# Kernel tuning notes

Hardware: AMD Instinct MI355X
Metric: run time of the kernel (lower is better)

Reference implementation:

```python
import jax, jax.numpy as jnp
import numpy as np

SEQ_LEN = 4096
N_FEAT = 2048
N_PADD = 128


def setup_inputs() -> dict:
    key = jax.random.key(0)
    kx, kw = jax.random.split(key)
    x = jax.random.normal(kx, (SEQ_LEN, N_FEAT), dtype=jnp.float32)
    # Fused QKV dense: features = 3 * n_feat
    W = jax.random.normal(kw, (N_FEAT, 3 * N_FEAT), dtype=jnp.float32) * (1.0 / np.sqrt(N_FEAT))
    b = jnp.zeros((3 * N_FEAT,), dtype=jnp.float32)
    return {"x": x, "W": W, "b": b, "n_padd": N_PADD}


def reference(x, W, b, n_padd):
    # Fused QKV projection, split along feature axis (as in nn.Dense + jnp.split)
    qkv = x @ W + b  # [S, 3F]
    q, k, v = jnp.split(qkv, 3, axis=1)  # each [S, F]
    S, F = q.shape
    idx = jnp.arange(S)
    # scores[i, j] = q_i . k_j / sqrt(F)
    scores = (q @ k.T) * (1.0 / jnp.sqrt(jnp.float32(F)))  # [S, S]
    seq_mask = idx >= n_padd                      # valid (non-padding) positions
    causal = idx[None, :] <= idx[:, None]         # j <= i
    mask = causal & seq_mask[None, :]             # kernel: causal_mask & seq_mask
    row_valid = seq_mask                          # rows < n_padd are not computed/stored
    neg_inf = jnp.float32(-jnp.inf)
    scores = jnp.where(mask, scores, neg_inf)
    # Fully-masked (padding) rows would softmax to NaN; neutralize then zero output.
    scores = jnp.where(row_valid[:, None], scores, 0.0)
    att = jax.nn.softmax(scores, axis=-1)         # row-wise stable softmax
    out = att @ v                                 # [S, F]
    out = jnp.where(row_valid[:, None], out, 0.0)  # padded rows produce zeros
    return out
```

## Files before the change

### kernel.cpp

```cpp
#include <hip/hip_runtime.h>
#include <cstdint>
#include <cstddef>
#include <cmath>

typedef unsigned short u16;
typedef short v8s __attribute__((ext_vector_type(8)));
typedef float v4f __attribute__((ext_vector_type(4)));

constexpr int SEQ = 4096;
constexpr int FEAT = 2048;
constexpr int F3 = 6144;


__device__ __forceinline__ u16 f2bf(float f) {
  union { float f; uint32_t u; } v; v.f = f;
  uint32_t r = v.u + 0x7FFFu + ((v.u >> 16) & 1u);
  return (u16)(r >> 16);
}

__device__ __forceinline__ float bf2f(u16 s) {
  union { uint32_t u; float f; } v; v.u = ((uint32_t)s) << 16;
  return v.f;
}

__device__ __forceinline__ void gld_lds16(const u16* g, u16* l) {
  __builtin_amdgcn_global_load_lds(
      (const __attribute__((address_space(1))) void*)g,
      (__attribute__((address_space(3))) void*)l, 16, 0, 0);
}


__global__ void cvt_f32_bf16(const float* __restrict__ in, u16* __restrict__ out, int n8) {
  int i = blockIdx.x * 256 + threadIdx.x;
  if (i >= n8) return;
  const float4* p = (const float4*)in + (size_t)i * 2;
  float4 a = p[0], b = p[1];
  union { u16 s[8]; uint4 v; } u;
  u.s[0] = f2bf(a.x); u.s[1] = f2bf(a.y); u.s[2] = f2bf(a.z); u.s[3] = f2bf(a.w);
  u.s[4] = f2bf(b.x); u.s[5] = f2bf(b.y); u.s[6] = f2bf(b.z); u.s[7] = f2bf(b.w);
  *(uint4*)(out + (size_t)i * 8) = u.v;
}

__global__ void transp_f2b(const float* __restrict__ in, int ldin,
                           u16* __restrict__ out, int ldout) {
  __shared__ float tile[32][33];
  int c0 = blockIdx.x * 32, r0 = blockIdx.y * 32;
  int tx = threadIdx.x, ty = threadIdx.y;
#pragma unroll
  for (int p = 0; p < 4; ++p)
    tile[ty + 8 * p][tx] = in[(size_t)(r0 + ty + 8 * p) * ldin + c0 + tx];
  __syncthreads();
#pragma unroll
  for (int p = 0; p < 4; ++p)
    out[(size_t)(c0 + ty + 8 * p) * ldout + r0 + tx] = f2bf(tile[tx][ty + 8 * p]);
}

__global__ void transp_b2b(const u16* __restrict__ in, int ldin,
                           u16* __restrict__ out, int ldout) {
  __shared__ u16 tile[32][33];
  int c0 = blockIdx.x * 32, r0 = blockIdx.y * 32;
  int tx = threadIdx.x, ty = threadIdx.y;
#pragma unroll
  for (int p = 0; p < 4; ++p)
    tile[ty + 8 * p][tx] = in[(size_t)(r0 + ty + 8 * p) * ldin + c0 + tx];
  __syncthreads();
#pragma unroll
  for (int p = 0; p < 4; ++p)
    out[(size_t)(c0 + ty + 8 * p) * ldout + r0 + tx] = tile[tx][ty + 8 * p];
}

__global__ __launch_bounds__(256) void add2_f32(
    const float* __restrict__ a, const float* __restrict__ b,
    float* __restrict__ o, int n4) {
  int i = blockIdx.x * 256 + threadIdx.x;
  if (i >= n4) return;
  float4 x = ((const float4*)a)[i], y = ((const float4*)b)[i];
  x.x += y.x; x.y += y.y; x.z += y.z; x.w += y.w;
  ((float4*)o)[i] = x;
}


#define BARW() asm volatile("s_barrier" ::: "memory")
#define VMC6() asm volatile("s_waitcnt vmcnt(6)" ::: "memory")
#define LGKM0() asm volatile("s_waitcnt lgkmcnt(0)" ::: "memory")

#define STAGE(SB, KO) do { \
  u16* Lb = &LDSU[SB][0] + w * 512; \
  gld_lds16(pA0 + (KO), Lb); \
  gld_lds16(pA0 + (size_t)64 * LDA_ + (KO), Lb + 2048); \
  gld_lds16(pB0 + (KO), Lb + 4096); \
  gld_lds16(pB0 + (size_t)64 * LDB_ + (KO), Lb + 4096 + 2048); \
  gld_lds16(pB0 + (size_t)128 * LDB_ + (KO), Lb + 4096 + 4096); \
  gld_lds16(pB0 + (size_t)192 * LDB_ + (KO), Lb + 4096 + 6144); \
} while (0)

#define LOADA(BUF) do { _Pragma("unroll") \
  for (int mi = 0; mi < 8; ++mi) \
    af[mi] = *(const v8s*)(&LDSU[BUF][0] + (mi * 16 + lm) * 32 + lqs); \
} while (0)

#define LOADB(BUF) do { _Pragma("unroll") \
  for (int ni = 0; ni < 4; ++ni) \
    bf4[ni] = *(const v8s*)(&LDSU[BUF][0] + 4096 + (w * 64 + ni * 16 + lm) * 32 + lqs); \
} while (0)

template<int LDA_, int LDB_, int LDC_, int OUTMODE ,
         int ADDB, int MODE, int SWZ>
__global__ __launch_bounds__(256, 2) void gemmw(
    const u16* __restrict__ A, const u16* __restrict__ B,
    void* __restrict__ Cv, int K,
    const float* __restrict__ bias, float scale) {
  int bi, bj, ks, ke;
  if (MODE == 1) {
    const int f = blockIdx.x;
    const int r = f & 255;
    const int h = f >> 8;
    const int g = r >> 4;
    bi = h ? g : 31 - g;
    const int idx = r & 15;
    bj = idx >> 1;
    const int z = idx & 1;
    const int kq = (bi + 1) * 64;
    ks = z ? kq : 0;  ke = ks + kq;
    Cv = (void*)((float*)Cv + (size_t)z * SEQ * FEAT);
  } else {
    if (SWZ) {
      const int gx = gridDim.x, gy = gridDim.y;
      const int b = blockIdx.y * gx + blockIdx.x;
      const int cpx = (gx * gy) >> 3;
      const int s = (b & 7) * cpx + (b >> 3);
      bi = s % gy;  bj = s / gy;
    } else { bj = blockIdx.x; bi = blockIdx.y; }
    ks = 0; ke = K;
  }
  const int i0 = bi * 128, j0 = bj * 256;

  __shared__ u16 LDSU[3][12288];

  const int t = threadIdx.x;
  const int w = t >> 6, l = t & 63;
  const int lm = l & 15, lq = l >> 4;
  const int lqs = ((lq + (lm >> 1)) & 3) * 8;

  const int rA = w * 16 + (l >> 2);
  const int cA = ((((l & 3) - ((rA >> 1) & 3)) & 3)) * 8;
  const u16* pA0 = A + (size_t)(i0 + rA) * LDA_ + cA;
  const u16* pB0 = B + (size_t)(j0 + rA) * LDB_ + cA;

  v4f acc[8][4];
#pragma unroll
  for (int a = 0; a < 8; ++a)
#pragma unroll
    for (int b2 = 0; b2 < 4; ++b2)
      acc[a][b2] = v4f{0.f, 0.f, 0.f, 0.f};

  v8s af[8], bf4[4];

  STAGE(0, ks); STAGE(1, ks + 32);
  VMC6(); BARW();
  LOADB(0);

  const int nt = (ke - ks) >> 5;
  int b0 = 0, b1 = 1;
  for (int tt = 0; tt < nt; tt += 2) {
    const int kc = ks + (tt << 5);
    const int s2 = 3 - b0 - b1;
    {
      const int kst = (kc + 64 < ke) ? kc + 64 : ks;
      STAGE(s2, kst);
      LOADA(b0);
      __builtin_amdgcn_s_setprio(1);
#pragma unroll
      for (int mi = 0; mi < 8; ++mi)
#pragma unroll
        for (int ni = 0; ni < 4; ++ni)
          acc[mi][ni] = __builtin_amdgcn_mfma_f32_16x16x32_bf16(af[mi], bf4[ni], acc[mi][ni], 0, 0, 0);
      __builtin_amdgcn_s_setprio(0);
      VMC6(); BARW();
      LOADB(b1);
    }
    {
      const int kst = (kc + 96 < ke) ? kc + 96 : ks;
      STAGE(b0, kst);
      LOADA(b1);
      __builtin_amdgcn_s_setprio(1);
#pragma unroll
      for (int mi = 0; mi < 8; ++mi)
#pragma unroll
        for (int ni = 0; ni < 4; ++ni)
          acc[mi][ni] = __builtin_amdgcn_mfma_f32_16x16x32_bf16(af[mi], bf4[ni], acc[mi][ni], 0, 0, 0);
      __builtin_amdgcn_s_setprio(0);
      VMC6(); BARW();
      LOADB(s2);
    }
    b1 = b0; b0 = s2;
  }

#pragma unroll
  for (int mi = 0; mi < 8; ++mi) {
#pragma unroll
    for (int ni = 0; ni < 4; ++ni) {
      const int cc = j0 + w * 64 + ni * 16 + lm;
      const float badd = ADDB ? bias[cc] : 0.f;
#pragma unroll
      for (int r = 0; r < 4; ++r) {
        const int rr = i0 + mi * 16 + lq * 4 + r;
        if (OUTMODE == 0)
          ((u16*)Cv)[(size_t)rr * LDC_ + cc] = f2bf(acc[mi][ni][r] * scale + badd);
        else
          ((float*)Cv)[(size_t)rr * LDC_ + cc] = acc[mi][ni][r];
      }
    }
  }
}

#undef STAGE
#undef LOADA
#undef LOADB


#define LDA8(BUF, MH) do { _Pragma("unroll") \
  for (int fi = 0; fi < 4; ++fi) { \
    const u16* ap = &As8[BUF][wr][(MH) * 4096 + fi * 1024]; \
    af[fi][0] = *(const v8s*)(ap + off0); \
    af[fi][1] = *(const v8s*)(ap + off1); \
  } } while (0)

#define LDB8(BUF) do { _Pragma("unroll") \
  for (int ni = 0; ni < 4; ++ni) { \
    const u16* bp = &Bs8[BUF][bh][bo + ni * 1024]; \
    bfr[ni][0] = *(const v8s*)(bp + off0); \
    bfr[ni][1] = *(const v8s*)(bp + off1); \
  } } while (0)

#define MMA8(MH, NL) do { _Pragma("unroll") \
  for (int fi = 0; fi < 4; ++fi) { _Pragma("unroll") \
    for (int nn = 0; nn < 2; ++nn) { \
      acc[(MH)*4+fi][(NL)+nn] = __builtin_amdgcn_mfma_f32_16x16x32_bf16( \
          af[fi][0], bfr[(NL)+nn][0], acc[(MH)*4+fi][(NL)+nn], 0, 0, 0); \
      acc[(MH)*4+fi][(NL)+nn] = __builtin_amdgcn_mfma_f32_16x16x32_bf16( \
          af[fi][1], bfr[(NL)+nn][1], acc[(MH)*4+fi][(NL)+nn], 0, 0, 0); \
    } } } while (0)

#define STG8A(BUF, H, KO) do { \
  gld_lds16(Ag + (size_t)(H) * 128 * LDA_ + (KO), &As8[BUF][H][w8 * 1024]); \
  gld_lds16(Ag + ((size_t)(H) * 128 + 8) * LDA_ + (KO), &As8[BUF][H][w8 * 1024 + 512]); \
  } while (0)

#define STG8B(BUF, H, KO) do { \
  gld_lds16(Bg + (size_t)(H) * 128 * LDB_ + (KO), &Bs8[BUF][H][w8 * 1024]); \
  gld_lds16(Bg + ((size_t)(H) * 128 + 8) * LDB_ + (KO), &Bs8[BUF][H][w8 * 1024 + 512]); \
  } while (0)

template<int LDA_, int LDB_, int LDC_>
__global__ __launch_bounds__(512, 2) void gemm8tri(
    const u16* __restrict__ A, const u16* __restrict__ B,
    u16* __restrict__ C, int K, float scale) {
  const int b = blockIdx.x;
  const int cpx = (int)gridDim.x >> 3;
  const int s = (b & 7) * cpx + (b >> 3);
  int bi = (int)((sqrtf(8.f * s + 1.f) - 1.f) * 0.5f);
  while ((bi + 1) * (bi + 2) / 2 <= s) ++bi;
  while (bi * (bi + 1) / 2 > s) --bi;
  const int bj = s - bi * (bi + 1) / 2;
  const int i0 = bi * 256, j0 = bj * 256;

  __shared__ u16 As8[2][2][8192];
  __shared__ u16 Bs8[2][2][8192];

  const int t = threadIdx.x;
  const int w8 = t >> 6, l = t & 63;
  const int wr = w8 >> 2, wc = w8 & 3;
  const int lm = l & 15, lq = l >> 4;
  const int bh = wc >> 1, bo = (wc & 1) * 4096;

  const int off0 = lm * 64 + ((lq + lm) & 7) * 8;
  const int off1 = lm * 64 + ((lq + lm + 4) & 7) * 8;

  const int srow = w8 * 16 + (l >> 3);
  const int scol = (((l & 7) - (l >> 3)) & 7) * 8;
  const u16* Ag = A + (size_t)(i0 + srow) * LDA_ + scol;
  const u16* Bg = B + (size_t)(j0 + srow) * LDB_ + scol;

  v4f acc[8][4];
#pragma unroll
  for (int a = 0; a < 8; ++a)
#pragma unroll
    for (int b2 = 0; b2 < 4; ++b2)
      acc[a][b2] = v4f{0.f, 0.f, 0.f, 0.f};

  v8s af[4][2], bfr[4][2];

  STG8B(0, 0, 0); STG8B(0, 1, 0); STG8A(0, 0, 0); STG8A(0, 1, 0);
  STG8B(1, 0, 64); STG8B(1, 1, 64); STG8A(1, 0, 64);
  VMC6(); BARW();

  const int nit = K >> 7;
  for (int it = 0; it < nit; ++it) {
    const int kc = it << 7;
    const int k1 = kc + 64;
    int k2 = kc + 128; if (k2 >= K) k2 = 0;
    int k3 = kc + 192; if (k3 >= K) k3 = 0;

    LDA8(0, 0); LDB8(0);
    STG8A(1, 1, k1);
    BARW(); LGKM0();
    __builtin_amdgcn_s_setprio(1); MMA8(0, 0); __builtin_amdgcn_s_setprio(0);
    BARW();
    STG8B(0, 0, k2);
    BARW();
    __builtin_amdgcn_s_setprio(1); MMA8(0, 2); __builtin_amdgcn_s_setprio(0);
    BARW();
    LDA8(0, 1);
    STG8B(0, 1, k2);
    BARW(); LGKM0();
    __builtin_amdgcn_s_setprio(1); MMA8(1, 0); __builtin_amdgcn_s_setprio(0);
    BARW();
    STG8A(0, 0, k2);
    BARW();
    __builtin_amdgcn_s_setprio(1); MMA8(1, 2); __builtin_amdgcn_s_setprio(0);
    VMC6(); BARW();
    LDA8(1, 0); LDB8(1);
    STG8A(0, 1, k2);
    BARW(); LGKM0();
    __builtin_amdgcn_s_setprio(1); MMA8(0, 0); __builtin_amdgcn_s_setprio(0);
    BARW();
    STG8B(1, 0, k3);
    BARW();
    __builtin_amdgcn_s_setprio(1); MMA8(0, 2); __builtin_amdgcn_s_setprio(0);
    BARW();
    LDA8(1, 1);
    STG8B(1, 1, k3);
    BARW(); LGKM0();
    __builtin_amdgcn_s_setprio(1); MMA8(1, 0); __builtin_amdgcn_s_setprio(0);
    BARW();
    STG8A(1, 0, k3);
    BARW();
    __builtin_amdgcn_s_setprio(1); MMA8(1, 2); __builtin_amdgcn_s_setprio(0);
    VMC6(); BARW();
  }

#pragma unroll
  for (int mi = 0; mi < 8; ++mi) {
#pragma unroll
    for (int ni = 0; ni < 4; ++ni) {
      const int cc = j0 + wc * 64 + ni * 16 + lm;
#pragma unroll
      for (int r = 0; r < 4; ++r) {
        const int rr = i0 + wr * 128 + mi * 16 + lq * 4 + r;
        C[(size_t)rr * LDC_ + cc] = f2bf(acc[mi][ni][r] * scale);
      }
    }
  }
}

#undef LDA8
#undef LDB8
#undef MMA8
#undef STG8A
#undef STG8B

__global__ __launch_bounds__(256) void softmax_rows(
    const u16* __restrict__ S0,
    u16* __restrict__ att, const int* __restrict__ npad_p) {
  const int i = blockIdx.x;
  const int np = *npad_p;
  const int kend = ((i >> 7) + 1) << 7;
  const u16* r0 = S0 + (size_t)i * SEQ;
  u16* arow = att + (size_t)i * SEQ;
  const int t = threadIdx.x;

  float m = -3.0e38f, s = 0.f;
  for (int j = np + t; j <= i; j += 256) {
    float v = bf2f(r0[j]);
    if (v > m) { s = s * __expf(m - v) + 1.f; m = v; }
    else       { s += __expf(v - m); }
  }
#pragma unroll
  for (int off = 32; off > 0; off >>= 1) {
    float mo = __shfl_xor(m, off);
    float so = __shfl_xor(s, off);
    float M = fmaxf(m, mo);
    s = s * __expf(m - M) + so * __expf(mo - M);
    m = M;
  }
  __shared__ float sm[4], ss[4];
  const int w = t >> 6, l = t & 63;
  if (l == 0) { sm[w] = m; ss[w] = s; }
  __syncthreads();
  const float M = fmaxf(fmaxf(sm[0], sm[1]), fmaxf(sm[2], sm[3]));
  const float Ssum = ss[0] * __expf(sm[0] - M) + ss[1] * __expf(sm[1] - M) +
                     ss[2] * __expf(sm[2] - M) + ss[3] * __expf(sm[3] - M);
  const float inv = 1.f / Ssum;

  for (int j0b = t * 8; j0b < kend; j0b += 2048) {
    union { u16 s8[8]; uint4 v; } u;
#pragma unroll
    for (int q = 0; q < 8; ++q) {
      const int j = j0b + q;
      float a = 0.f;
      if (j >= np && j <= i)
        a = __expf(bf2f(r0[j]) - M) * inv;
      u.s8[q] = f2bf(a);
    }
    *(uint4*)(arow + j0b) = u.v;
  }
}


extern "C" void kernel_launch(void* const* d_in, const int* in_sizes, int n_in,
                              void* d_out, int out_size, void* d_ws, size_t ws_size,
                              hipStream_t stream) {
  const float* x = (const float*)d_in[0];
  const float* W = (const float*)d_in[1];
  const float* b = (const float*)d_in[2];
  const int* npad = (const int*)d_in[3];
  float* out = (float*)d_out;

  char* p = (char*)d_ws;
  u16* xb = (u16*)p;
  u16* Wt = (u16*)(p + (size_t)SEQ * FEAT * 2);
  u16* att = (u16*)p;
  p += (size_t)SEQ * FEAT * 2 + (size_t)F3 * FEAT * 2;
  u16* qkvb = (u16*)p;  p += (size_t)SEQ * F3 * 2;
  u16* vt   = (u16*)p;  p += (size_t)FEAT * SEQ * 2;
  u16* sc0  = (u16*)p;  p += (size_t)SEQ * SEQ * 2;
  p += (size_t)SEQ * SEQ * 2;
  if (ws_size < (size_t)(p - (char*)d_ws)) return;

  float* p0 = (float*)sc0;
  float* p1 = p0 + (size_t)SEQ * FEAT;

  const float scale = 0.02209708691207961f;

  cvt_f32_bf16<<<SEQ * FEAT / 8 / 256, 256, 0, stream>>>(x, xb, SEQ * FEAT / 8);
  transp_f2b<<<dim3(F3 / 32, FEAT / 32), dim3(32, 8), 0, stream>>>(W, F3, Wt, FEAT);
  gemmw<FEAT, FEAT, F3, 0, 1, 0, 1><<<dim3(F3 / 256, SEQ / 128), 256, 0, stream>>>(
      xb, Wt, (void*)qkvb, FEAT, b, 1.0f);
  transp_b2b<<<dim3(FEAT / 32, SEQ / 32), dim3(32, 8), 0, stream>>>(
      qkvb + 2 * FEAT, F3, vt, SEQ);
  gemm8tri<F3, F3, SEQ><<<dim3(136), 512, 0, stream>>>(
      qkvb, qkvb + FEAT, sc0, FEAT, scale);
  softmax_rows<<<SEQ, 256, 0, stream>>>(sc0, att, npad);
  gemmw<SEQ, SEQ, FEAT, 1, 0, 1, 0><<<dim3(512), 256, 0, stream>>>(
      att, vt, (void*)p0, 0, nullptr, 1.0f);
  add2_f32<<<SEQ * FEAT / 4 / 256, 256, 0, stream>>>(p0, p1, out, SEQ * FEAT / 4);
}
```

Measured before the change: 375.7 us.

## Vectorize softmax row loads and remap split-K block order in att@V GEMM

The softmax kernel now reads scores as 16-byte uint4 vectors of 8 bf16 values in both the max/sum pass and the normalize pass, replacing scalar 2-byte loads. The online max/sum update now runs per element inside the unrolled inner loop under a causal/padding guard. The MODE 1 (split-K causal att@V) GEMM block index mapping is reordered so the two K-halves split across grid halves, and consecutive blocks alternate between long and short rows across column tiles. This aims to balance work and improve L2 locality, at the cost of a different scheduling pattern.

```diff
diff --git a/kernel.cpp b/kernel.cpp
--- a/kernel.cpp
+++ b/kernel.cpp
@@ -113,13 +113,12 @@
   int bi, bj, ks, ke;
   if (MODE == 1) {
     const int f = blockIdx.x;
-    const int r = f & 255;
-    const int h = f >> 8;
-    const int g = r >> 4;
-    bi = h ? g : 31 - g;
-    const int idx = r & 15;
-    bj = idx >> 1;
-    const int z = idx & 1;
+    const int d3 = (f >> 3) & 1;
+    const int par = (f & 1) ^ d3;
+    const int p = (f >> 4) & 15;
+    const int z = f >> 8;
+    bi = par ? p : 31 - p;
+    bj = ((f >> 1) & 3) | (d3 << 2);
     const int kq = (bi + 1) * 64;
     ks = z ? kq : 0;  ke = ks + kq;
     Cv = (void*)((float*)Cv + (size_t)z * SEQ * FEAT);
@@ -371,10 +370,18 @@
   const int t = threadIdx.x;
 
   float m = -3.0e38f, s = 0.f;
-  for (int j = np + t; j <= i; j += 256) {
-    float v = bf2f(r0[j]);
-    if (v > m) { s = s * __expf(m - v) + 1.f; m = v; }
-    else       { s += __expf(v - m); }
+  for (int j0b = t * 8; j0b < kend; j0b += 2048) {
+    union { u16 s8[8]; uint4 v; } ui;
+    ui.v = *(const uint4*)(r0 + j0b);
+#pragma unroll
+    for (int q = 0; q < 8; ++q) {
+      const int j = j0b + q;
+      if (j >= np && j <= i) {
+        const float v = bf2f(ui.s8[q]);
+        if (v > m) { s = s * __expf(m - v) + 1.f; m = v; }
+        else       { s += __expf(v - m); }
+      }
+    }
   }
 #pragma unroll
   for (int off = 32; off > 0; off >>= 1) {
@@ -394,16 +401,17 @@
   const float inv = 1.f / Ssum;
 
   for (int j0b = t * 8; j0b < kend; j0b += 2048) {
-    union { u16 s8[8]; uint4 v; } u;
+    union { u16 s8[8]; uint4 v; } ui, uo;
+    ui.v = *(const uint4*)(r0 + j0b);
 #pragma unroll
     for (int q = 0; q < 8; ++q) {
       const int j = j0b + q;
       float a = 0.f;
       if (j >= np && j <= i)
-        a = __expf(bf2f(r0[j]) - M) * inv;
-      u.s8[q] = f2bf(a);
-    }
-    *(uint4*)(arow + j0b) = u.v;
+        a = __expf(bf2f(ui.s8[q]) - M) * inv;
+      uo.s8[q] = f2bf(a);
+    }
+    *(uint4*)(arow + j0b) = uo.v;
   }
 }
 
```

Measured after the change: 391.8 us. +4.3%, slower.
